# Performance work log

Measured on AMD Instinct MI355X. Metric: run time of the kernel, lower is better.

The kernel has to match this reference:

```python
import jax, jax.numpy as jnp
import numpy as np

OBS, ACT, H = 64, 16, 64
T, B = 512, 4096


def _orth(key, shape):
    # orthogonal init like nn.init.orthogonal_ (gain 1 for predict; capture uses
    # gain sqrt(2) via init_ wrapper, but predict re-inits to plain orthogonal).
    a = jax.random.normal(key, shape, dtype=jnp.float32)
    q, r = jnp.linalg.qr(a if shape[0] >= shape[1] else a.T)
    q = q * jnp.sign(jnp.diag(r))
    return q if shape[0] >= shape[1] else q.T


def setup_inputs() -> dict:
    key = jax.random.key(0)
    ks = jax.random.split(key, 10)
    g2 = np.sqrt(2.0).astype(np.float32)
    inp = {
        "x": jax.random.normal(ks[0], (T, B, OBS), dtype=jnp.float32),
        "h": jax.random.normal(ks[1], (1, B, H), dtype=jnp.float32),
        "g": jax.random.uniform(ks[2], (T, B, 1), dtype=jnp.float32),
        "a": jax.random.normal(ks[3], (T, B, ACT), dtype=jnp.float32),
        # capture MLP: Linear(obs->H), tanh, Linear(H->H), tanh  (gain sqrt(2))
        "Wc1": g2 * _orth(ks[4], (OBS, H)),
        "bc1": jnp.zeros((H,), jnp.float32),
        "Wc2": g2 * _orth(ks[5], (H, H)),
        "bc2": jnp.zeros((H,), jnp.float32),
        # predict (Dynamics): Linear(H+ACT->H), tanh, Linear(H->H), tanh (gain 1)
        "Wp1": _orth(ks[6], (H + ACT, H)),
        "bp1": jnp.zeros((H,), jnp.float32),
        "Wp2": _orth(ks[7], (H, H)),
        "bp2": jnp.zeros((H,), jnp.float32),
    }
    return inp


def reference(x, h, g, a, Wc1, bc1, Wc2, bc2, Wp1, bp1, Wp2, bp2):
    # capture branch has no recurrent dependence -> compute for all t at once
    z1_all = jnp.tanh(jnp.tanh(x @ Wc1 + bc1) @ Wc2 + bc2)  # [T, B, H]

    def step(h_prev, inp):  # h_prev: [B, H]
        z1_t, g_t, a_t = inp
        ha = jnp.concatenate([h_prev, a_t], axis=-1)  # [B, H+ACT]
        z2 = jnp.tanh(jnp.tanh(ha @ Wp1 + bp1) @ Wp2 + bp2)
        h_new = (1.0 - g_t) * z1_t + g_t * z2
        return h_new, h_new

    h_final, outs = jax.lax.scan(step, h[0], (z1_all, g, a))
    capt = z1_all.reshape(-1, z1_all.shape[-1])  # torch.cat over [B,H] chunks -> [T*B, H]
    return outs, h_final[None], capt
```

## Files before the change

kernel.cpp:

```cpp
#include <hip/hip_runtime.h>
#include <hip/hip_bf16.h>

#define T_STEPS 512
#define BATCH   4096
#define ACT     16
#define HDIM    64

typedef short s8v __attribute__((ext_vector_type(8)));
typedef float f4v __attribute__((ext_vector_type(4)));

#define MFMA16(A, B, C) __builtin_amdgcn_mfma_f32_16x16x32_bf16((A), (B), (C), 0, 0, 0)

__device__ __forceinline__ unsigned pkbf(float a, float b) {
    unsigned r;
    asm("v_cvt_pk_bf16_f32 %0, %1, %2" : "=v"(r) : "v"(a), "v"(b));
    return r;
}
__device__ __forceinline__ float hi16f(unsigned p) { return __builtin_bit_cast(float, p & 0xFFFF0000u); }
__device__ __forceinline__ unsigned short f2bf(float f) {
    unsigned u = __builtin_bit_cast(unsigned, f);
    u += 0x7FFFu + ((u >> 16) & 1u);
    return (unsigned short)(u >> 16);
}
__device__ __forceinline__ float bf2f(unsigned short b) {
    return __builtin_bit_cast(float, ((unsigned)b) << 16);
}
__device__ __forceinline__ float ftanh(float x) {
    float e = __expf(2.0f * x);
    return fmaf(-2.0f, __builtin_amdgcn_rcpf(e + 1.0f), 1.0f);
}
struct i4x { int a, b, c, d; };
__device__ __forceinline__ s8v pack4(f4v v) {
    unsigned p0 = pkbf(v[0], v[0]); float r0 = v[0] - hi16f(p0);
    unsigned p1 = pkbf(v[1], v[1]); float r1 = v[1] - hi16f(p1);
    unsigned p2 = pkbf(v[2], v[2]); float r2 = v[2] - hi16f(p2);
    unsigned p3 = pkbf(v[3], v[3]); float r3 = v[3] - hi16f(p3);
    i4x w{(int)pkbf(v[0], r0), (int)pkbf(v[1], r1), (int)pkbf(v[2], r2), (int)pkbf(v[3], r3)};
    return __builtin_bit_cast(s8v, w);
}
#define BAR() do { \
    asm volatile("s_waitcnt lgkmcnt(0)" ::: "memory"); \
    __builtin_amdgcn_s_barrier(); \
    asm volatile("" ::: "memory"); \
} while (0)

__global__ __launch_bounds__(256, 1) void capture_k(
    const float* __restrict__ x,
    const float* __restrict__ Wc1, const float* __restrict__ bc1,
    const float* __restrict__ Wc2, const float* __restrict__ bc2,
    float* __restrict__ capt)
{
    const int tid = threadIdx.x;
    const int l   = tid & 63;
    const int m   = l & 15;
    const int q   = l >> 4;
    const int gw  = blockIdx.x * 4 + (tid >> 6);
    const int NW  = 1024;
    const long NT = (long)T_STEPS * BATCH / 16;

    s8v C1[4][4], C2h[4][4], C2l[4][4];
    f4v d1v[4], d2v[4];
    #pragma unroll
    for (int T = 0; T < 4; ++T) {
        #pragma unroll
        for (int f = 0; f < 4; ++f) {
            #pragma unroll
            for (int e = 0; e < 8; ++e) {
                const int j = f * 16 + q * 4 + (e >> 1);
                C1[T][f][e] = (short)f2bf(Wc1[j * 64 + 16 * T + m]);
                float v2 = Wc2[j * 64 + 16 * T + m];
                unsigned short h2 = f2bf(v2);
                C2h[T][f][e] = (short)h2;
                C2l[T][f][e] = (short)f2bf(v2 - bf2f(h2));
            }
        }
        d1v[T] = *(const f4v*)&bc1[16 * T + 4 * q];
        d2v[T] = *(const f4v*)&bc2[16 * T + 4 * q];
    }

    long tile = gw;
    if (tile >= NT) return;
    f4v XC[4];
    #pragma unroll
    for (int f = 0; f < 4; ++f)
        XC[f] = *(const f4v*)&x[(tile * 16 + m) * 64 + 16 * f + 4 * q];

    for (; tile < NT; tile += NW) {
        const long nxt = (tile + NW < NT) ? tile + NW : tile;
        f4v XN[4];
        #pragma unroll
        for (int f = 0; f < 4; ++f)
            XN[f] = *(const f4v*)&x[(nxt * 16 + m) * 64 + 16 * f + 4 * q];

        s8v xf[4];
        #pragma unroll
        for (int f = 0; f < 4; ++f) xf[f] = pack4(XC[f]);

        s8v tcf[4];
        #pragma unroll
        for (int T = 0; T < 4; ++T) {
            f4v u0 = d1v[T];
            f4v u1 = {0.f, 0.f, 0.f, 0.f};
            u0 = MFMA16(C1[T][0], xf[0], u0);
            u1 = MFMA16(C1[T][1], xf[1], u1);
            u0 = MFMA16(C1[T][2], xf[2], u0);
            u1 = MFMA16(C1[T][3], xf[3], u1);
            f4v tv;
            #pragma unroll
            for (int r = 0; r < 4; ++r) tv[r] = ftanh(u0[r] + u1[r]);
            tcf[T] = pack4(tv);
        }
        #pragma unroll
        for (int T = 0; T < 4; ++T) {
            f4v c0 = d2v[T];
            f4v c1 = {0.f, 0.f, 0.f, 0.f}, c2 = c1, c3 = c1;
            c0 = MFMA16(C2h[T][0], tcf[0], c0);
            c1 = MFMA16(C2h[T][1], tcf[1], c1);
            c2 = MFMA16(C2h[T][2], tcf[2], c2);
            c3 = MFMA16(C2h[T][3], tcf[3], c3);
            c0 = MFMA16(C2l[T][0], tcf[0], c0);
            c1 = MFMA16(C2l[T][1], tcf[1], c1);
            c2 = MFMA16(C2l[T][2], tcf[2], c2);
            c3 = MFMA16(C2l[T][3], tcf[3], c3);
            f4v zv;
            #pragma unroll
            for (int r = 0; r < 4; ++r) zv[r] = ftanh((c0[r] + c1[r]) + (c2[r] + c3[r]));
            *(f4v*)&capt[(tile * 16 + m) * 64 + 16 * T + 4 * q] = zv;
        }
        #pragma unroll
        for (int f = 0; f < 4; ++f) XC[f] = XN[f];
    }
}

__global__ __launch_bounds__(256, 1) void recur_k(
    const float* __restrict__ h0, const float* __restrict__ g,
    const float* __restrict__ a,  const float* __restrict__ Wp1,
    const float* __restrict__ bp1, const float* __restrict__ Wp2,
    const float* __restrict__ bp2, const float* __restrict__ z1,
    float* __restrict__ outs, float* __restrict__ hfin)
{
    __shared__ s8v hx[4][64];
    __shared__ s8v t1x[4][64];

    const int tid = threadIdx.x;
    const int T   = tid >> 6;
    const int l   = tid & 63;
    const int m   = l & 15;
    const int q   = l >> 4;
    const int b0  = blockIdx.x << 4;

    s8v W1[5], W2h[4], W2l[4];
    #pragma unroll
    for (int f = 0; f < 4; ++f) {
        #pragma unroll
        for (int e = 0; e < 8; ++e) {
            const int j = f * 16 + q * 4 + (e >> 1);
            W1[f][e] = (short)f2bf(Wp1[j * 64 + 16 * T + m]);
            float v2 = Wp2[j * 64 + 16 * T + m];
            unsigned short h2 = f2bf(v2);
            W2h[f][e] = (short)h2;
            W2l[f][e] = (short)f2bf(v2 - bf2f(h2));
        }
    }
    #pragma unroll
    for (int e = 0; e < 8; ++e) {
        const int j = 64 + q * 4 + (e >> 1);
        W1[4][e] = (short)f2bf(Wp1[j * 64 + 16 * T + m]);
    }
    const f4v b1v = *(const f4v*)&bp1[16 * T + 4 * q];
    const f4v b2v = *(const f4v*)&bp2[16 * T + 4 * q];

    const long zoff = (long)(b0 + m) * 64 + 16 * T + 4 * q;
    const long aoff = (long)(b0 + m) * ACT + 4 * q;
    const long goff = (long)(b0 + m);

    {
        f4v h0v = *(const f4v*)&h0[zoff];
        hx[T][l] = pack4(h0v);
    }
    f4v zP0 = *(const f4v*)&z1[0 * (long)BATCH * 64 + zoff];
    f4v zP1 = *(const f4v*)&z1[1 * (long)BATCH * 64 + zoff];
    f4v zP2 = *(const f4v*)&z1[2 * (long)BATCH * 64 + zoff];
    f4v zP3 = *(const f4v*)&z1[3 * (long)BATCH * 64 + zoff];
    f4v aP0 = *(const f4v*)&a[0 * (long)BATCH * ACT + aoff];
    f4v aP1 = *(const f4v*)&a[1 * (long)BATCH * ACT + aoff];
    f4v aP2 = *(const f4v*)&a[2 * (long)BATCH * ACT + aoff];
    f4v aP3 = *(const f4v*)&a[3 * (long)BATCH * ACT + aoff];
    float gP0 = g[0 * (long)BATCH + goff];
    float gP1 = g[1 * (long)BATCH + goff];
    float gP2 = g[2 * (long)BATCH + goff];
    float gP3 = g[3 * (long)BATCH + goff];

    float* outp = &outs[zoff];
    f4v hl = {0.f, 0.f, 0.f, 0.f};
    __syncthreads();

#define RSTEP(tt, ZP, AP, GP) {                                               \
                                    \
    s8v hf0 = hx[0][l];                                                       \
    s8v hf1 = hx[1][l];                                                       \
    s8v hf2 = hx[2][l];                                                       \
    s8v hf3 = hx[3][l];                                                       \
    s8v afr = pack4(AP);                                                      \
    f4v p0 = b1v;                                                             \
    f4v p1 = {0.f, 0.f, 0.f, 0.f}, p2 = p1;                                   \
    p0 = MFMA16(W1[0], hf0, p0);                                              \
    p1 = MFMA16(W1[1], hf1, p1);                                              \
    p2 = MFMA16(W1[2], hf2, p2);                                              \
    p0 = MFMA16(W1[3], hf3, p0);                                              \
    p1 = MFMA16(W1[4], afr, p1);                                              \
    f4v tv;                                                                   \
    _Pragma("unroll")                                                         \
    for (int r = 0; r < 4; ++r) tv[r] = ftanh((p0[r] + p1[r]) + p2[r]);       \
    t1x[T][l] = pack4(tv);                                                    \
    BAR();                                                                    \
                                           \
    s8v tf0 = t1x[0][l];                                                      \
    s8v tf1 = t1x[1][l];                                                      \
    s8v tf2 = t1x[2][l];                                                      \
    s8v tf3 = t1x[3][l];                                                      \
    f4v c0 = b2v;                                                             \
    f4v c1 = {0.f, 0.f, 0.f, 0.f}, c2 = c1, c3 = c1;                          \
    c0 = MFMA16(W2h[0], tf0, c0);                                             \
    c1 = MFMA16(W2h[1], tf1, c1);                                             \
    c2 = MFMA16(W2h[2], tf2, c2);                                             \
    c3 = MFMA16(W2h[3], tf3, c3);                                             \
    c0 = MFMA16(W2l[0], tf0, c0);                                             \
    c1 = MFMA16(W2l[1], tf1, c1);                                             \
    c2 = MFMA16(W2l[2], tf2, c2);                                             \
    c3 = MFMA16(W2l[3], tf3, c3);                                             \
    f4v hv;                                                                   \
    _Pragma("unroll")                                                         \
    for (int r = 0; r < 4; ++r) {                                             \
        float z2 = ftanh((c0[r] + c1[r]) + (c2[r] + c3[r]));                  \
        hv[r] = fmaf(GP, z2 - ZP[r], ZP[r]);                                  \
    }                                                                         \
    *(f4v*)outp = hv;                                                         \
    outp += (long)BATCH * HDIM;                                               \
    hl = hv;                                                                  \
    hx[T][l] = pack4(hv);                                                     \
                                     \
    {                                                                         \
        const long tn = ((tt) + 4 < T_STEPS) ? (tt) + 4 : T_STEPS - 1;        \
        ZP = *(const f4v*)&z1[tn * (long)BATCH * 64 + zoff];                  \
        AP = *(const f4v*)&a[tn * (long)BATCH * ACT + aoff];                  \
        GP = g[tn * (long)BATCH + goff];                                      \
    }                                                                         \
    BAR();                                                                    \
}

    for (int t = 0; t < T_STEPS; t += 4) {
        RSTEP(t + 0, zP0, aP0, gP0);
        RSTEP(t + 1, zP1, aP1, gP1);
        RSTEP(t + 2, zP2, aP2, gP2);
        RSTEP(t + 3, zP3, aP3, gP3);
    }
#undef RSTEP

    *(f4v*)&hfin[zoff] = hl;
}

extern "C" void kernel_launch(void* const* d_in, const int* in_sizes, int n_in,
                              void* d_out, int out_size, void* d_ws, size_t ws_size,
                              hipStream_t stream) {
    const float* x   = (const float*)d_in[0];
    const float* h0  = (const float*)d_in[1];
    const float* g   = (const float*)d_in[2];
    const float* a   = (const float*)d_in[3];
    const float* Wc1 = (const float*)d_in[4];
    const float* bc1 = (const float*)d_in[5];
    const float* Wc2 = (const float*)d_in[6];
    const float* bc2 = (const float*)d_in[7];
    const float* Wp1 = (const float*)d_in[8];
    const float* bp1 = (const float*)d_in[9];
    const float* Wp2 = (const float*)d_in[10];
    const float* bp2 = (const float*)d_in[11];

    float* outs = (float*)d_out;
    float* hfin = outs + (long)T_STEPS * BATCH * HDIM;
    float* capt = hfin + (long)BATCH * HDIM;

    capture_k<<<256, 256, 0, stream>>>(x, Wc1, bc1, Wc2, bc2, capt);
    recur_k<<<BATCH / 16, 256, 0, stream>>>(h0, g, a, Wp1, bp1, Wp2, bp2, capt, outs, hfin);
}
```

Baseline: 605.0 us.

## Fuse capture MLP and recurrence into one warp-specialized kernel with LDS flag handoff

Merges the two kernels into one 512-thread block. Four producer waves compute the capture MLP and pass z1 through a 4-deep LDS ring, so z1 is no longer re-read from global memory by the recurrence. Four consumer waves each compute the full first predict layer redundantly, which removes the mid-step barrier, and they double-buffer h. The two wave groups synchronize with volatile LDS flags and s_sleep spin-waits instead of block barriers. The risks are spin-wait overhead, more registers per wave, and the correctness of the flag ordering.

```diff
diff --git a/kernel.cpp b/kernel.cpp
--- a/kernel.cpp
+++ b/kernel.cpp
@@ -38,226 +38,242 @@
     i4x w{(int)pkbf(v[0], r0), (int)pkbf(v[1], r1), (int)pkbf(v[2], r2), (int)pkbf(v[3], r3)};
     return __builtin_bit_cast(s8v, w);
 }
-#define BAR() do { \
-    asm volatile("s_waitcnt lgkmcnt(0)" ::: "memory"); \
-    __builtin_amdgcn_s_barrier(); \
-    asm volatile("" ::: "memory"); \
-} while (0)
-
-__global__ __launch_bounds__(256, 1) void capture_k(
-    const float* __restrict__ x,
+
+__global__ __launch_bounds__(512, 2) void fused_cell(
+    const float* __restrict__ x,  const float* __restrict__ h0,
+    const float* __restrict__ g,  const float* __restrict__ a,
     const float* __restrict__ Wc1, const float* __restrict__ bc1,
     const float* __restrict__ Wc2, const float* __restrict__ bc2,
-    float* __restrict__ capt)
+    const float* __restrict__ Wp1, const float* __restrict__ bp1,
+    const float* __restrict__ Wp2, const float* __restrict__ bp2,
+    float* __restrict__ outs, float* __restrict__ hfin, float* __restrict__ capt)
 {
+    __shared__ s8v   hx[2][4][64];
+    __shared__ float zr[4][16][68];
+    __shared__ int   flg[16];
+
     const int tid = threadIdx.x;
-    const int l   = tid & 63;
-    const int m   = l & 15;
-    const int q   = l >> 4;
-    const int gw  = blockIdx.x * 4 + (tid >> 6);
-    const int NW  = 1024;
-    const long NT = (long)T_STEPS * BATCH / 16;
-
-    s8v C1[4][4], C2h[4][4], C2l[4][4];
-    f4v d1v[4], d2v[4];
-    #pragma unroll
-    for (int T = 0; T < 4; ++T) {
+    const int wv  = tid >> 6;
+    const int T   = wv & 3;
+    const bool capw = wv >= 4;
+    const int l  = tid & 63;
+    const int m  = l & 15;
+    const int q  = l >> 4;
+    const int b0 = blockIdx.x << 4;
+
+    volatile int* pf = (volatile int*)flg;
+    volatile int* zf = (volatile int*)(flg + 8);
+    if (tid < 16) flg[tid] = 0;
+
+    if (!capw) {
+        s8v W1[4][5];
+        s8v W2h[4], W2l[4];
+        f4v b1v[4], b2v;
         #pragma unroll
-        for (int f = 0; f < 4; ++f) {
+        for (int o = 0; o < 4; ++o) {
+            #pragma unroll
+            for (int f = 0; f < 4; ++f)
+                #pragma unroll
+                for (int e = 0; e < 8; ++e) {
+                    const int j = f * 16 + q * 4 + (e >> 1);
+                    W1[o][f][e] = (short)f2bf(Wp1[j * 64 + 16 * o + m]);
+                }
+            #pragma unroll
+            for (int e = 0; e < 8; ++e) {
+                const int j = 64 + q * 4 + (e >> 1);
+                W1[o][4][e] = (short)f2bf(Wp1[j * 64 + 16 * o + m]);
+            }
+            b1v[o] = *(const f4v*)&bp1[16 * o + 4 * q];
+        }
+        #pragma unroll
+        for (int f = 0; f < 4; ++f)
             #pragma unroll
             for (int e = 0; e < 8; ++e) {
                 const int j = f * 16 + q * 4 + (e >> 1);
-                C1[T][f][e] = (short)f2bf(Wc1[j * 64 + 16 * T + m]);
-                float v2 = Wc2[j * 64 + 16 * T + m];
+                float v2 = Wp2[j * 64 + 16 * T + m];
                 unsigned short h2 = f2bf(v2);
-                C2h[T][f][e] = (short)h2;
-                C2l[T][f][e] = (short)f2bf(v2 - bf2f(h2));
+                W2h[f][e] = (short)h2;
+                W2l[f][e] = (short)f2bf(v2 - bf2f(h2));
             }
-        }
-        d1v[T] = *(const f4v*)&bc1[16 * T + 4 * q];
-        d2v[T] = *(const f4v*)&bc2[16 * T + 4 * q];
-    }
-
-    long tile = gw;
-    if (tile >= NT) return;
-    f4v XC[4];
-    #pragma unroll
-    for (int f = 0; f < 4; ++f)
-        XC[f] = *(const f4v*)&x[(tile * 16 + m) * 64 + 16 * f + 4 * q];
-
-    for (; tile < NT; tile += NW) {
-        const long nxt = (tile + NW < NT) ? tile + NW : tile;
-        f4v XN[4];
-        #pragma unroll
-        for (int f = 0; f < 4; ++f)
-            XN[f] = *(const f4v*)&x[(nxt * 16 + m) * 64 + 16 * f + 4 * q];
-
-        s8v xf[4];
-        #pragma unroll
-        for (int f = 0; f < 4; ++f) xf[f] = pack4(XC[f]);
-
-        s8v tcf[4];
-        #pragma unroll
-        for (int T = 0; T < 4; ++T) {
-            f4v u0 = d1v[T];
-            f4v u1 = {0.f, 0.f, 0.f, 0.f};
-            u0 = MFMA16(C1[T][0], xf[0], u0);
-            u1 = MFMA16(C1[T][1], xf[1], u1);
-            u0 = MFMA16(C1[T][2], xf[2], u0);
-            u1 = MFMA16(C1[T][3], xf[3], u1);
-            f4v tv;
-            #pragma unroll
-            for (int r = 0; r < 4; ++r) tv[r] = ftanh(u0[r] + u1[r]);
-            tcf[T] = pack4(tv);
-        }
-        #pragma unroll
-        for (int T = 0; T < 4; ++T) {
-            f4v c0 = d2v[T];
-            f4v c1 = {0.f, 0.f, 0.f, 0.f}, c2 = c1, c3 = c1;
-            c0 = MFMA16(C2h[T][0], tcf[0], c0);
-            c1 = MFMA16(C2h[T][1], tcf[1], c1);
-            c2 = MFMA16(C2h[T][2], tcf[2], c2);
-            c3 = MFMA16(C2h[T][3], tcf[3], c3);
-            c0 = MFMA16(C2l[T][0], tcf[0], c0);
-            c1 = MFMA16(C2l[T][1], tcf[1], c1);
-            c2 = MFMA16(C2l[T][2], tcf[2], c2);
-            c3 = MFMA16(C2l[T][3], tcf[3], c3);
-            f4v zv;
-            #pragma unroll
-            for (int r = 0; r < 4; ++r) zv[r] = ftanh((c0[r] + c1[r]) + (c2[r] + c3[r]));
-            *(f4v*)&capt[(tile * 16 + m) * 64 + 16 * T + 4 * q] = zv;
-        }
-        #pragma unroll
-        for (int f = 0; f < 4; ++f) XC[f] = XN[f];
-    }
-}
-
-__global__ __launch_bounds__(256, 1) void recur_k(
-    const float* __restrict__ h0, const float* __restrict__ g,
-    const float* __restrict__ a,  const float* __restrict__ Wp1,
-    const float* __restrict__ bp1, const float* __restrict__ Wp2,
-    const float* __restrict__ bp2, const float* __restrict__ z1,
-    float* __restrict__ outs, float* __restrict__ hfin)
-{
-    __shared__ s8v hx[4][64];
-    __shared__ s8v t1x[4][64];
-
-    const int tid = threadIdx.x;
-    const int T   = tid >> 6;
-    const int l   = tid & 63;
-    const int m   = l & 15;
-    const int q   = l >> 4;
-    const int b0  = blockIdx.x << 4;
-
-    s8v W1[5], W2h[4], W2l[4];
-    #pragma unroll
-    for (int f = 0; f < 4; ++f) {
-        #pragma unroll
-        for (int e = 0; e < 8; ++e) {
-            const int j = f * 16 + q * 4 + (e >> 1);
-            W1[f][e] = (short)f2bf(Wp1[j * 64 + 16 * T + m]);
-            float v2 = Wp2[j * 64 + 16 * T + m];
-            unsigned short h2 = f2bf(v2);
-            W2h[f][e] = (short)h2;
-            W2l[f][e] = (short)f2bf(v2 - bf2f(h2));
-        }
-    }
-    #pragma unroll
-    for (int e = 0; e < 8; ++e) {
-        const int j = 64 + q * 4 + (e >> 1);
-        W1[4][e] = (short)f2bf(Wp1[j * 64 + 16 * T + m]);
-    }
-    const f4v b1v = *(const f4v*)&bp1[16 * T + 4 * q];
-    const f4v b2v = *(const f4v*)&bp2[16 * T + 4 * q];
-
-    const long zoff = (long)(b0 + m) * 64 + 16 * T + 4 * q;
-    const long aoff = (long)(b0 + m) * ACT + 4 * q;
-    const long goff = (long)(b0 + m);
-
-    {
-        f4v h0v = *(const f4v*)&h0[zoff];
-        hx[T][l] = pack4(h0v);
-    }
-    f4v zP0 = *(const f4v*)&z1[0 * (long)BATCH * 64 + zoff];
-    f4v zP1 = *(const f4v*)&z1[1 * (long)BATCH * 64 + zoff];
-    f4v zP2 = *(const f4v*)&z1[2 * (long)BATCH * 64 + zoff];
-    f4v zP3 = *(const f4v*)&z1[3 * (long)BATCH * 64 + zoff];
-    f4v aP0 = *(const f4v*)&a[0 * (long)BATCH * ACT + aoff];
-    f4v aP1 = *(const f4v*)&a[1 * (long)BATCH * ACT + aoff];
-    f4v aP2 = *(const f4v*)&a[2 * (long)BATCH * ACT + aoff];
-    f4v aP3 = *(const f4v*)&a[3 * (long)BATCH * ACT + aoff];
-    float gP0 = g[0 * (long)BATCH + goff];
-    float gP1 = g[1 * (long)BATCH + goff];
-    float gP2 = g[2 * (long)BATCH + goff];
-    float gP3 = g[3 * (long)BATCH + goff];
-
-    float* outp = &outs[zoff];
-    f4v hl = {0.f, 0.f, 0.f, 0.f};
-    __syncthreads();
-
-#define RSTEP(tt, ZP, AP, GP) {                                               \
-                                    \
-    s8v hf0 = hx[0][l];                                                       \
-    s8v hf1 = hx[1][l];                                                       \
-    s8v hf2 = hx[2][l];                                                       \
-    s8v hf3 = hx[3][l];                                                       \
-    s8v afr = pack4(AP);                                                      \
-    f4v p0 = b1v;                                                             \
-    f4v p1 = {0.f, 0.f, 0.f, 0.f}, p2 = p1;                                   \
-    p0 = MFMA16(W1[0], hf0, p0);                                              \
-    p1 = MFMA16(W1[1], hf1, p1);                                              \
-    p2 = MFMA16(W1[2], hf2, p2);                                              \
-    p0 = MFMA16(W1[3], hf3, p0);                                              \
-    p1 = MFMA16(W1[4], afr, p1);                                              \
-    f4v tv;                                                                   \
+        b2v = *(const f4v*)&bp2[16 * T + 4 * q];
+
+        hx[0][T][l] = pack4(*(const f4v*)&h0[(long)(b0 + m) * 64 + 16 * T + 4 * q]);
+
+        const long aoff = (long)(b0 + m) * ACT + 4 * q;
+        const long goff = (long)(b0 + m);
+        f4v aA = *(const f4v*)&a[aoff];
+        f4v aB = *(const f4v*)&a[(long)BATCH * ACT + aoff];
+        float gA = g[goff];
+        float gB = g[(long)BATCH + goff];
+        const float* apA = a + (long)2 * BATCH * ACT + aoff;
+        const float* apB = a + (long)3 * BATCH * ACT + aoff;
+        const float* gpA = g + (long)2 * BATCH + goff;
+        const float* gpB = g + (long)3 * BATCH + goff;
+
+        float* outp = &outs[(long)(b0 + m) * 64 + 16 * T + 4 * q];
+        f4v hl = {0.f, 0.f, 0.f, 0.f};
+
+        __syncthreads();
+        __builtin_amdgcn_s_setprio(1);
+
+#define L1T(o, dst) {                                                         \
+    f4v p0 = b1v[o];                                                          \
+    f4v p1 = {0.f, 0.f, 0.f, 0.f};                                            \
+    p0 = MFMA16(W1[o][0], hf0, p0);                                           \
+    p1 = MFMA16(W1[o][1], hf1, p1);                                           \
+    p0 = MFMA16(W1[o][2], hf2, p0);                                           \
+    p1 = MFMA16(W1[o][3], hf3, p1);                                           \
+    p0 = MFMA16(W1[o][4], afr, p0);                                           \
+    f4v tv_;                                                                  \
     _Pragma("unroll")                                                         \
-    for (int r = 0; r < 4; ++r) tv[r] = ftanh((p0[r] + p1[r]) + p2[r]);       \
-    t1x[T][l] = pack4(tv);                                                    \
-    BAR();                                                                    \
-                                           \
-    s8v tf0 = t1x[0][l];                                                      \
-    s8v tf1 = t1x[1][l];                                                      \
-    s8v tf2 = t1x[2][l];                                                      \
-    s8v tf3 = t1x[3][l];                                                      \
+    for (int r = 0; r < 4; ++r) tv_[r] = ftanh(p0[r] + p1[r]);                \
+    dst = pack4(tv_);                                                         \
+}
+
+#define RSTEP(tt, AC, GC, APTR, GPTR) do {                                    \
+    const int t_ = (tt);                                                      \
+    const f4v aC_ = AC; const float gC_ = GC;                                 \
+    while (pf[0] < t_ || pf[1] < t_ || pf[2] < t_ || pf[3] < t_ ||            \
+           zf[0] <= t_ || zf[1] <= t_ || zf[2] <= t_ || zf[3] <= t_)          \
+        __builtin_amdgcn_s_sleep(1);                                          \
+    asm volatile("" ::: "memory");                                            \
+    const f4v z1v = *(const f4v*)&zr[t_ & 3][m][16 * T + 4 * q];              \
+    const s8v* hb = &hx[t_ & 1][0][0];                                        \
+    const s8v hf0 = hb[l];                                                    \
+    const s8v hf1 = hb[64 + l];                                               \
+    const s8v hf2 = hb[128 + l];                                              \
+    const s8v hf3 = hb[192 + l];                                              \
+    const s8v afr = pack4(aC_);                                               \
+    AC = *(const f4v*)APTR; if (t_ + 4 < T_STEPS) APTR += 2 * BATCH * ACT;    \
+    GC = *GPTR;             if (t_ + 4 < T_STEPS) GPTR += 2 * BATCH;          \
+    s8v tcf0, tcf1, tcf2, tcf3;                                               \
+    L1T(0, tcf0) L1T(1, tcf1) L1T(2, tcf2) L1T(3, tcf3)                       \
     f4v c0 = b2v;                                                             \
     f4v c1 = {0.f, 0.f, 0.f, 0.f}, c2 = c1, c3 = c1;                          \
-    c0 = MFMA16(W2h[0], tf0, c0);                                             \
-    c1 = MFMA16(W2h[1], tf1, c1);                                             \
-    c2 = MFMA16(W2h[2], tf2, c2);                                             \
-    c3 = MFMA16(W2h[3], tf3, c3);                                             \
-    c0 = MFMA16(W2l[0], tf0, c0);                                             \
-    c1 = MFMA16(W2l[1], tf1, c1);                                             \
-    c2 = MFMA16(W2l[2], tf2, c2);                                             \
-    c3 = MFMA16(W2l[3], tf3, c3);                                             \
+    c0 = MFMA16(W2h[0], tcf0, c0); c1 = MFMA16(W2h[1], tcf1, c1);             \
+    c2 = MFMA16(W2h[2], tcf2, c2); c3 = MFMA16(W2h[3], tcf3, c3);             \
+    c0 = MFMA16(W2l[0], tcf0, c0); c1 = MFMA16(W2l[1], tcf1, c1);             \
+    c2 = MFMA16(W2l[2], tcf2, c2); c3 = MFMA16(W2l[3], tcf3, c3);             \
     f4v hv;                                                                   \
     _Pragma("unroll")                                                         \
     for (int r = 0; r < 4; ++r) {                                             \
         float z2 = ftanh((c0[r] + c1[r]) + (c2[r] + c3[r]));                  \
-        hv[r] = fmaf(GP, z2 - ZP[r], ZP[r]);                                  \
+        hv[r] = fmaf(gC_, z2 - z1v[r], z1v[r]);                               \
     }                                                                         \
-    *(f4v*)outp = hv;                                                         \
-    outp += (long)BATCH * HDIM;                                               \
+    *(f4v*)outp = hv; outp += (long)BATCH * HDIM;                             \
     hl = hv;                                                                  \
-    hx[T][l] = pack4(hv);                                                     \
-                                     \
-    {                                                                         \
-        const long tn = ((tt) + 4 < T_STEPS) ? (tt) + 4 : T_STEPS - 1;        \
-        ZP = *(const f4v*)&z1[tn * (long)BATCH * 64 + zoff];                  \
-        AP = *(const f4v*)&a[tn * (long)BATCH * ACT + aoff];                  \
-        GP = g[tn * (long)BATCH + goff];                                      \
+    hx[(t_ + 1) & 1][T][l] = pack4(hv);                                       \
+    asm volatile("s_waitcnt lgkmcnt(0)" ::: "memory");                        \
+    if (l == 0) pf[T] = t_ + 1;                                               \
+} while (0)
+
+        for (int t = 0; t < T_STEPS; t += 2) {
+            RSTEP(t,     aA, gA, apA, gpA);
+            RSTEP(t + 1, aB, gB, apB, gpB);
+        }
+#undef RSTEP
+#undef L1T
+
+        *(f4v*)&hfin[(long)(b0 + m) * 64 + 16 * T + 4 * q] = hl;
+
+    } else {
+        s8v C1[4][4];
+        s8v C2h[4], C2l[4];
+        f4v d1v[4], d2v;
+        #pragma unroll
+        for (int o = 0; o < 4; ++o) {
+            #pragma unroll
+            for (int f = 0; f < 4; ++f)
+                #pragma unroll
+                for (int e = 0; e < 8; ++e) {
+                    const int j = f * 16 + q * 4 + (e >> 1);
+                    C1[o][f][e] = (short)f2bf(Wc1[j * 64 + 16 * o + m]);
+                }
+            d1v[o] = *(const f4v*)&bc1[16 * o + 4 * q];
+        }
+        #pragma unroll
+        for (int f = 0; f < 4; ++f)
+            #pragma unroll
+            for (int e = 0; e < 8; ++e) {
+                const int j = f * 16 + q * 4 + (e >> 1);
+                float v2 = Wc2[j * 64 + 16 * T + m];
+                unsigned short h2 = f2bf(v2);
+                C2h[f][e] = (short)h2;
+                C2l[f][e] = (short)f2bf(v2 - bf2f(h2));
+            }
+        d2v = *(const f4v*)&bc2[16 * T + 4 * q];
+
+        const float* bx = x + (long)(b0 + m) * 64 + 4 * q;
+        f4v XA0 = *(const f4v*)(bx);
+        f4v XA1 = *(const f4v*)(bx + 16);
+        f4v XA2 = *(const f4v*)(bx + 32);
+        f4v XA3 = *(const f4v*)(bx + 48);
+        const float* bx1 = bx + (long)BATCH * HDIM;
+        f4v XB0 = *(const f4v*)(bx1);
+        f4v XB1 = *(const f4v*)(bx1 + 16);
+        f4v XB2 = *(const f4v*)(bx1 + 32);
+        f4v XB3 = *(const f4v*)(bx1 + 48);
+        const float* xpA = bx + (long)2 * BATCH * HDIM;
+        const float* xpB = bx + (long)3 * BATCH * HDIM;
+
+        float* cp = &capt[(long)(b0 + m) * 64 + 16 * T + 4 * q];
+
+        __syncthreads();
+
+#define CL1T(o, dst) {                                                        \
+    f4v p0 = d1v[o];                                                          \
+    f4v p1 = {0.f, 0.f, 0.f, 0.f};                                            \
+    p0 = MFMA16(C1[o][0], xf0, p0);                                           \
+    p1 = MFMA16(C1[o][1], xf1, p1);                                           \
+    p0 = MFMA16(C1[o][2], xf2, p0);                                           \
+    p1 = MFMA16(C1[o][3], xf3, p1);                                           \
+    f4v tv_;                                                                  \
+    _Pragma("unroll")                                                         \
+    for (int r = 0; r < 4; ++r) tv_[r] = ftanh(p0[r] + p1[r]);                \
+    dst = pack4(tv_);                                                         \
+}
+
+#define CSTEP(tt, X0, X1, X2, X3, XPTR) do {                                  \
+    const int t_ = (tt);                                                      \
+    if (t_ >= 4) {                                                            \
+        const int want = t_ - 3;                                              \
+        while (pf[0] < want || pf[1] < want || pf[2] < want || pf[3] < want)  \
+            __builtin_amdgcn_s_sleep(1);                                      \
+        asm volatile("" ::: "memory");                                        \
     }                                                                         \
-    BAR();                                                                    \
-}
-
-    for (int t = 0; t < T_STEPS; t += 4) {
-        RSTEP(t + 0, zP0, aP0, gP0);
-        RSTEP(t + 1, zP1, aP1, gP1);
-        RSTEP(t + 2, zP2, aP2, gP2);
-        RSTEP(t + 3, zP3, aP3, gP3);
+    const s8v xf0 = pack4(X0);                                                \
+    const s8v xf1 = pack4(X1);                                                \
+    const s8v xf2 = pack4(X2);                                                \
+    const s8v xf3 = pack4(X3);                                                \
+    X0 = *(const f4v*)(XPTR);                                                 \
+    X1 = *(const f4v*)(XPTR + 16);                                            \
+    X2 = *(const f4v*)(XPTR + 32);                                            \
+    X3 = *(const f4v*)(XPTR + 48);                                            \
+    if (t_ + 4 < T_STEPS) XPTR += (long)2 * BATCH * HDIM;                     \
+    s8v tcf0, tcf1, tcf2, tcf3;                                               \
+    CL1T(0, tcf0) CL1T(1, tcf1) CL1T(2, tcf2) CL1T(3, tcf3)                   \
+    f4v c0 = d2v;                                                             \
+    f4v c1 = {0.f, 0.f, 0.f, 0.f}, c2 = c1, c3 = c1;                          \
+    c0 = MFMA16(C2h[0], tcf0, c0); c1 = MFMA16(C2h[1], tcf1, c1);             \
+    c2 = MFMA16(C2h[2], tcf2, c2); c3 = MFMA16(C2h[3], tcf3, c3);             \
+    c0 = MFMA16(C2l[0], tcf0, c0); c1 = MFMA16(C2l[1], tcf1, c1);             \
+    c2 = MFMA16(C2l[2], tcf2, c2); c3 = MFMA16(C2l[3], tcf3, c3);             \
+    f4v zv;                                                                   \
+    _Pragma("unroll")                                                         \
+    for (int r = 0; r < 4; ++r) zv[r] = ftanh((c0[r] + c1[r]) + (c2[r] + c3[r])); \
+    *(f4v*)&zr[t_ & 3][m][16 * T + 4 * q] = zv;                               \
+    *(f4v*)cp = zv; cp += (long)BATCH * HDIM;                                 \
+    asm volatile("s_waitcnt lgkmcnt(0)" ::: "memory");                        \
+    if (l == 0) zf[T] = t_ + 1;                                               \
+} while (0)
+
+        for (int t = 0; t < T_STEPS; t += 2) {
+            CSTEP(t,     XA0, XA1, XA2, XA3, xpA);
+            CSTEP(t + 1, XB0, XB1, XB2, XB3, xpB);
+        }
+#undef CSTEP
+#undef CL1T
     }
-#undef RSTEP
-
-    *(f4v*)&hfin[zoff] = hl;
 }
 
 extern "C" void kernel_launch(void* const* d_in, const int* in_sizes, int n_in,
@@ -280,6 +296,6 @@
     float* hfin = outs + (long)T_STEPS * BATCH * HDIM;
     float* capt = hfin + (long)BATCH * HDIM;
 
-    capture_k<<<256, 256, 0, stream>>>(x, Wc1, bc1, Wc2, bc2, capt);
-    recur_k<<<BATCH / 16, 256, 0, stream>>>(h0, g, a, Wp1, bp1, Wp2, bp2, capt, outs, hfin);
-}
+    fused_cell<<<BATCH / 16, 512, 0, stream>>>(
+        x, h0, g, a, Wc1, bc1, Wc2, bc2, Wp1, bp1, Wp2, bp2, outs, hfin, capt);
+}
```

New measurement: 1.003 ms. 1.66x slower.

## Process two batch tiles per recurrent block and double capture grid

Applied to the files above, without the earlier changes.

The recurrent kernel now has each block handle 32 batch rows as two independent 16-row chains. Their MFMAs are interleaved so each barrier and the tanh latency are shared across twice the work, and the launch uses half as many blocks (128). The prefetch distance drops from four steps to two to keep register pressure manageable. The capture kernel moves to 512 blocks with launch bounds allowing 2 blocks per CU, which raises occupancy but may increase register pressure. The risks are that 128 blocks leave many CUs idle and that the shorter prefetch distance exposes more load latency.

```diff
diff --git a/kernel.cpp b/kernel.cpp
--- a/kernel.cpp
+++ b/kernel.cpp
@@ -44,7 +44,7 @@
     asm volatile("" ::: "memory"); \
 } while (0)
 
-__global__ __launch_bounds__(256, 1) void capture_k(
+__global__ __launch_bounds__(256, 2) void capture_k(
     const float* __restrict__ x,
     const float* __restrict__ Wc1, const float* __restrict__ bc1,
     const float* __restrict__ Wc2, const float* __restrict__ bc2,
@@ -55,7 +55,7 @@
     const int m   = l & 15;
     const int q   = l >> 4;
     const int gw  = blockIdx.x * 4 + (tid >> 6);
-    const int NW  = 1024;
+    const int NW  = 2048;
     const long NT = (long)T_STEPS * BATCH / 16;
 
     s8v C1[4][4], C2h[4][4], C2l[4][4];
@@ -139,19 +139,19 @@
     const float* __restrict__ bp2, const float* __restrict__ z1,
     float* __restrict__ outs, float* __restrict__ hfin)
 {
-    __shared__ s8v hx[4][64];
-    __shared__ s8v t1x[4][64];
+    __shared__ s8v hx[2][4][64];
+    __shared__ s8v t1x[2][4][64];
 
     const int tid = threadIdx.x;
     const int T   = tid >> 6;
     const int l   = tid & 63;
     const int m   = l & 15;
     const int q   = l >> 4;
-    const int b0  = blockIdx.x << 4;
+    const int b0  = blockIdx.x << 5;
 
     s8v W1[5], W2h[4], W2l[4];
     #pragma unroll
-    for (int f = 0; f < 4; ++f) {
+    for (int f = 0; f < 4; ++f)
         #pragma unroll
         for (int e = 0; e < 8; ++e) {
             const int j = f * 16 + q * 4 + (e >> 1);
@@ -161,7 +161,6 @@
             W2h[f][e] = (short)h2;
             W2l[f][e] = (short)f2bf(v2 - bf2f(h2));
         }
-    }
     #pragma unroll
     for (int e = 0; e < 8; ++e) {
         const int j = 64 + q * 4 + (e >> 1);
@@ -170,94 +169,114 @@
     const f4v b1v = *(const f4v*)&bp1[16 * T + 4 * q];
     const f4v b2v = *(const f4v*)&bp2[16 * T + 4 * q];
 
-    const long zoff = (long)(b0 + m) * 64 + 16 * T + 4 * q;
-    const long aoff = (long)(b0 + m) * ACT + 4 * q;
-    const long goff = (long)(b0 + m);
-
-    {
-        f4v h0v = *(const f4v*)&h0[zoff];
-        hx[T][l] = pack4(h0v);
-    }
-    f4v zP0 = *(const f4v*)&z1[0 * (long)BATCH * 64 + zoff];
-    f4v zP1 = *(const f4v*)&z1[1 * (long)BATCH * 64 + zoff];
-    f4v zP2 = *(const f4v*)&z1[2 * (long)BATCH * 64 + zoff];
-    f4v zP3 = *(const f4v*)&z1[3 * (long)BATCH * 64 + zoff];
-    f4v aP0 = *(const f4v*)&a[0 * (long)BATCH * ACT + aoff];
-    f4v aP1 = *(const f4v*)&a[1 * (long)BATCH * ACT + aoff];
-    f4v aP2 = *(const f4v*)&a[2 * (long)BATCH * ACT + aoff];
-    f4v aP3 = *(const f4v*)&a[3 * (long)BATCH * ACT + aoff];
-    float gP0 = g[0 * (long)BATCH + goff];
-    float gP1 = g[1 * (long)BATCH + goff];
-    float gP2 = g[2 * (long)BATCH + goff];
-    float gP3 = g[3 * (long)BATCH + goff];
-
-    float* outp = &outs[zoff];
-    f4v hl = {0.f, 0.f, 0.f, 0.f};
+    const long zf0 = (long)(b0 + m) * 64 + 16 * T + 4 * q;
+    const long zf1 = zf0 + 16 * 64;
+    const long af0_ = (long)(b0 + m) * ACT + 4 * q;
+    const long af1_ = af0_ + 16 * ACT;
+    const long gf0 = (long)(b0 + m);
+    const long gf1 = gf0 + 16;
+
+    hx[0][T][l] = pack4(*(const f4v*)&h0[zf0]);
+    hx[1][T][l] = pack4(*(const f4v*)&h0[zf1]);
+
+    f4v z0A = *(const f4v*)&z1[zf0];
+    f4v z0B = *(const f4v*)&z1[(long)BATCH * 64 + zf0];
+    f4v z1A = *(const f4v*)&z1[zf1];
+    f4v z1B = *(const f4v*)&z1[(long)BATCH * 64 + zf1];
+    f4v a0A = *(const f4v*)&a[af0_];
+    f4v a0B = *(const f4v*)&a[(long)BATCH * ACT + af0_];
+    f4v a1A = *(const f4v*)&a[af1_];
+    f4v a1B = *(const f4v*)&a[(long)BATCH * ACT + af1_];
+    float g0A = g[gf0], g0B = g[(long)BATCH + gf0];
+    float g1A = g[gf1], g1B = g[(long)BATCH + gf1];
+
+    float* out0 = &outs[zf0];
+    float* out1 = &outs[zf1];
+    f4v hl0 = {0.f, 0.f, 0.f, 0.f}, hl1 = hl0;
     __syncthreads();
 
-#define RSTEP(tt, ZP, AP, GP) {                                               \
-                                    \
-    s8v hf0 = hx[0][l];                                                       \
-    s8v hf1 = hx[1][l];                                                       \
-    s8v hf2 = hx[2][l];                                                       \
-    s8v hf3 = hx[3][l];                                                       \
-    s8v afr = pack4(AP);                                                      \
-    f4v p0 = b1v;                                                             \
-    f4v p1 = {0.f, 0.f, 0.f, 0.f}, p2 = p1;                                   \
-    p0 = MFMA16(W1[0], hf0, p0);                                              \
-    p1 = MFMA16(W1[1], hf1, p1);                                              \
-    p2 = MFMA16(W1[2], hf2, p2);                                              \
-    p0 = MFMA16(W1[3], hf3, p0);                                              \
-    p1 = MFMA16(W1[4], afr, p1);                                              \
-    f4v tv;                                                                   \
-    _Pragma("unroll")                                                         \
-    for (int r = 0; r < 4; ++r) tv[r] = ftanh((p0[r] + p1[r]) + p2[r]);       \
-    t1x[T][l] = pack4(tv);                                                    \
-    BAR();                                                                    \
-                                           \
-    s8v tf0 = t1x[0][l];                                                      \
-    s8v tf1 = t1x[1][l];                                                      \
-    s8v tf2 = t1x[2][l];                                                      \
-    s8v tf3 = t1x[3][l];                                                      \
-    f4v c0 = b2v;                                                             \
-    f4v c1 = {0.f, 0.f, 0.f, 0.f}, c2 = c1, c3 = c1;                          \
-    c0 = MFMA16(W2h[0], tf0, c0);                                             \
-    c1 = MFMA16(W2h[1], tf1, c1);                                             \
-    c2 = MFMA16(W2h[2], tf2, c2);                                             \
-    c3 = MFMA16(W2h[3], tf3, c3);                                             \
-    c0 = MFMA16(W2l[0], tf0, c0);                                             \
-    c1 = MFMA16(W2l[1], tf1, c1);                                             \
-    c2 = MFMA16(W2l[2], tf2, c2);                                             \
-    c3 = MFMA16(W2l[3], tf3, c3);                                             \
-    f4v hv;                                                                   \
+#define RSTEP(tt, Z0, A0, G0, Z1v, A1, G1) do {                               \
+                                   \
+    const s8v h00 = hx[0][0][l];                                              \
+    const s8v h01 = hx[0][1][l];                                              \
+    const s8v h02 = hx[0][2][l];                                              \
+    const s8v h03 = hx[0][3][l];                                              \
+    const s8v h10 = hx[1][0][l];                                              \
+    const s8v h11 = hx[1][1][l];                                              \
+    const s8v h12 = hx[1][2][l];                                              \
+    const s8v h13 = hx[1][3][l];                                              \
+    const s8v af0 = pack4(A0);                                                \
+    const s8v af1 = pack4(A1);                                                \
+    f4v p00 = b1v, p10 = b1v;                                                 \
+    f4v p01 = {0.f, 0.f, 0.f, 0.f}, p02 = p01, p11 = p01, p12 = p01;          \
+    p00 = MFMA16(W1[0], h00, p00);  p10 = MFMA16(W1[0], h10, p10);            \
+    p01 = MFMA16(W1[1], h01, p01);  p11 = MFMA16(W1[1], h11, p11);            \
+    p02 = MFMA16(W1[2], h02, p02);  p12 = MFMA16(W1[2], h12, p12);            \
+    p00 = MFMA16(W1[3], h03, p00);  p10 = MFMA16(W1[3], h13, p10);            \
+    p01 = MFMA16(W1[4], af0, p01);  p11 = MFMA16(W1[4], af1, p11);            \
+    f4v tv0, tv1;                                                             \
     _Pragma("unroll")                                                         \
     for (int r = 0; r < 4; ++r) {                                             \
-        float z2 = ftanh((c0[r] + c1[r]) + (c2[r] + c3[r]));                  \
-        hv[r] = fmaf(GP, z2 - ZP[r], ZP[r]);                                  \
+        tv0[r] = ftanh((p00[r] + p01[r]) + p02[r]);                           \
+        tv1[r] = ftanh((p10[r] + p11[r]) + p12[r]);                           \
     }                                                                         \
-    *(f4v*)outp = hv;                                                         \
-    outp += (long)BATCH * HDIM;                                               \
-    hl = hv;                                                                  \
-    hx[T][l] = pack4(hv);                                                     \
-                                     \
+    t1x[0][T][l] = pack4(tv0);                                                \
+    t1x[1][T][l] = pack4(tv1);                                                \
+    BAR();                                                                    \
+                           \
+    const s8v t00 = t1x[0][0][l];                                             \
+    const s8v t01 = t1x[0][1][l];                                             \
+    const s8v t02 = t1x[0][2][l];                                             \
+    const s8v t03 = t1x[0][3][l];                                             \
+    const s8v t10 = t1x[1][0][l];                                             \
+    const s8v t11 = t1x[1][1][l];                                             \
+    const s8v t12 = t1x[1][2][l];                                             \
+    const s8v t13 = t1x[1][3][l];                                             \
+    f4v c00 = b2v, c10 = b2v;                                                 \
+    f4v c01 = {0.f, 0.f, 0.f, 0.f}, c02 = c01, c03 = c01;                     \
+    f4v c11 = c01, c12 = c01, c13 = c01;                                      \
+    c00 = MFMA16(W2h[0], t00, c00);  c10 = MFMA16(W2h[0], t10, c10);          \
+    c01 = MFMA16(W2h[1], t01, c01);  c11 = MFMA16(W2h[1], t11, c11);          \
+    c02 = MFMA16(W2h[2], t02, c02);  c12 = MFMA16(W2h[2], t12, c12);          \
+    c03 = MFMA16(W2h[3], t03, c03);  c13 = MFMA16(W2h[3], t13, c13);          \
+    c00 = MFMA16(W2l[0], t00, c00);  c10 = MFMA16(W2l[0], t10, c10);          \
+    c01 = MFMA16(W2l[1], t01, c01);  c11 = MFMA16(W2l[1], t11, c11);          \
+    c02 = MFMA16(W2l[2], t02, c02);  c12 = MFMA16(W2l[2], t12, c12);          \
+    c03 = MFMA16(W2l[3], t03, c03);  c13 = MFMA16(W2l[3], t13, c13);          \
+    f4v hv0, hv1;                                                             \
+    _Pragma("unroll")                                                         \
+    for (int r = 0; r < 4; ++r) {                                             \
+        float z20 = ftanh((c00[r] + c01[r]) + (c02[r] + c03[r]));             \
+        float z21 = ftanh((c10[r] + c11[r]) + (c12[r] + c13[r]));             \
+        hv0[r] = fmaf(G0, z20 - Z0[r], Z0[r]);                                \
+        hv1[r] = fmaf(G1, z21 - Z1v[r], Z1v[r]);                              \
+    }                                                                         \
+    *(f4v*)out0 = hv0;  out0 += (long)BATCH * HDIM;                           \
+    *(f4v*)out1 = hv1;  out1 += (long)BATCH * HDIM;                           \
+    hl0 = hv0; hl1 = hv1;                                                     \
+    hx[0][T][l] = pack4(hv0);                                                 \
+    hx[1][T][l] = pack4(hv1);                                                 \
+                                          \
     {                                                                         \
-        const long tn = ((tt) + 4 < T_STEPS) ? (tt) + 4 : T_STEPS - 1;        \
-        ZP = *(const f4v*)&z1[tn * (long)BATCH * 64 + zoff];                  \
-        AP = *(const f4v*)&a[tn * (long)BATCH * ACT + aoff];                  \
-        GP = g[tn * (long)BATCH + goff];                                      \
+        const long tn = ((tt) + 2 < T_STEPS) ? (tt) + 2 : T_STEPS - 1;        \
+        Z0  = *(const f4v*)&z1[tn * (long)BATCH * 64 + zf0];                  \
+        Z1v = *(const f4v*)&z1[tn * (long)BATCH * 64 + zf1];                  \
+        A0  = *(const f4v*)&a[tn * (long)BATCH * ACT + af0_];                 \
+        A1  = *(const f4v*)&a[tn * (long)BATCH * ACT + af1_];                 \
+        G0  = g[tn * (long)BATCH + gf0];                                      \
+        G1  = g[tn * (long)BATCH + gf1];                                      \
     }                                                                         \
     BAR();                                                                    \
-}
-
-    for (int t = 0; t < T_STEPS; t += 4) {
-        RSTEP(t + 0, zP0, aP0, gP0);
-        RSTEP(t + 1, zP1, aP1, gP1);
-        RSTEP(t + 2, zP2, aP2, gP2);
-        RSTEP(t + 3, zP3, aP3, gP3);
+} while (0)
+
+    for (int t = 0; t < T_STEPS; t += 2) {
+        RSTEP(t,     z0A, a0A, g0A, z1A, a1A, g1A);
+        RSTEP(t + 1, z0B, a0B, g0B, z1B, a1B, g1B);
     }
 #undef RSTEP
 
-    *(f4v*)&hfin[zoff] = hl;
+    *(f4v*)&hfin[zf0] = hl0;
+    *(f4v*)&hfin[zf1] = hl1;
 }
 
 extern "C" void kernel_launch(void* const* d_in, const int* in_sizes, int n_in,
@@ -280,6 +299,6 @@
     float* hfin = outs + (long)T_STEPS * BATCH * HDIM;
     float* capt = hfin + (long)BATCH * HDIM;
 
-    capture_k<<<256, 256, 0, stream>>>(x, Wc1, bc1, Wc2, bc2, capt);
-    recur_k<<<BATCH / 16, 256, 0, stream>>>(h0, g, a, Wp1, bp1, Wp2, bp2, capt, outs, hfin);
-}
+    capture_k<<<512, 256, 0, stream>>>(x, Wc1, bc1, Wc2, bc2, capt);
+    recur_k<<<BATCH / 32, 256, 0, stream>>>(h0, g, a, Wp1, bp1, Wp2, bp2, capt, outs, hfin);
+}
```

New measurement: 1.160 ms. 91.7% more time.

## Compute full first layer redundantly per wave to drop one barrier per step

Applied to the files above, without the earlier changes.

Each wave now computes all four 16-column tiles of the first predict layer (holding all W1 fragments in registers) instead of one tile, so the intermediate activation never goes through shared memory. This removes one of the two block barriers per recurrent step, and the hidden state buffer is double-buffered by step parity so a single barrier suffices. The trade-off is four times the layer-1 MFMA and tanh work per wave and higher register pressure from the extra weight fragments.

```diff
diff --git a/kernel.cpp b/kernel.cpp
--- a/kernel.cpp
+++ b/kernel.cpp
@@ -139,8 +139,7 @@
     const float* __restrict__ bp2, const float* __restrict__ z1,
     float* __restrict__ outs, float* __restrict__ hfin)
 {
-    __shared__ s8v hx[4][64];
-    __shared__ s8v t1x[4][64];
+    __shared__ s8v hx[2][4][64];
 
     const int tid = threadIdx.x;
     const int T   = tid >> 6;
@@ -149,35 +148,43 @@
     const int q   = l >> 4;
     const int b0  = blockIdx.x << 4;
 
-    s8v W1[5], W2h[4], W2l[4];
-    #pragma unroll
-    for (int f = 0; f < 4; ++f) {
+    s8v W1a[4][5];
+    f4v b1v[4];
+    #pragma unroll
+    for (int o = 0; o < 4; ++o) {
+        #pragma unroll
+        for (int f = 0; f < 4; ++f)
+            #pragma unroll
+            for (int e = 0; e < 8; ++e) {
+                const int j = f * 16 + q * 4 + (e >> 1);
+                W1a[o][f][e] = (short)f2bf(Wp1[j * 64 + 16 * o + m]);
+            }
+        #pragma unroll
+        for (int e = 0; e < 8; ++e) {
+            const int j = 64 + q * 4 + (e >> 1);
+            W1a[o][4][e] = (short)f2bf(Wp1[j * 64 + 16 * o + m]);
+        }
+        b1v[o] = *(const f4v*)&bp1[16 * o + 4 * q];
+    }
+    s8v W2h[4], W2l[4];
+    #pragma unroll
+    for (int f = 0; f < 4; ++f)
         #pragma unroll
         for (int e = 0; e < 8; ++e) {
             const int j = f * 16 + q * 4 + (e >> 1);
-            W1[f][e] = (short)f2bf(Wp1[j * 64 + 16 * T + m]);
             float v2 = Wp2[j * 64 + 16 * T + m];
             unsigned short h2 = f2bf(v2);
             W2h[f][e] = (short)h2;
             W2l[f][e] = (short)f2bf(v2 - bf2f(h2));
         }
-    }
-    #pragma unroll
-    for (int e = 0; e < 8; ++e) {
-        const int j = 64 + q * 4 + (e >> 1);
-        W1[4][e] = (short)f2bf(Wp1[j * 64 + 16 * T + m]);
-    }
-    const f4v b1v = *(const f4v*)&bp1[16 * T + 4 * q];
     const f4v b2v = *(const f4v*)&bp2[16 * T + 4 * q];
 
     const long zoff = (long)(b0 + m) * 64 + 16 * T + 4 * q;
     const long aoff = (long)(b0 + m) * ACT + 4 * q;
     const long goff = (long)(b0 + m);
 
-    {
-        f4v h0v = *(const f4v*)&h0[zoff];
-        hx[T][l] = pack4(h0v);
-    }
+    hx[0][T][l] = pack4(*(const f4v*)&h0[zoff]);
+
     f4v zP0 = *(const f4v*)&z1[0 * (long)BATCH * 64 + zoff];
     f4v zP1 = *(const f4v*)&z1[1 * (long)BATCH * 64 + zoff];
     f4v zP2 = *(const f4v*)&z1[2 * (long)BATCH * 64 + zoff];
@@ -186,49 +193,41 @@
     f4v aP1 = *(const f4v*)&a[1 * (long)BATCH * ACT + aoff];
     f4v aP2 = *(const f4v*)&a[2 * (long)BATCH * ACT + aoff];
     f4v aP3 = *(const f4v*)&a[3 * (long)BATCH * ACT + aoff];
-    float gP0 = g[0 * (long)BATCH + goff];
-    float gP1 = g[1 * (long)BATCH + goff];
-    float gP2 = g[2 * (long)BATCH + goff];
-    float gP3 = g[3 * (long)BATCH + goff];
+    float gP0 = g[0 * (long)BATCH + goff], gP1 = g[1 * (long)BATCH + goff];
+    float gP2 = g[2 * (long)BATCH + goff], gP3 = g[3 * (long)BATCH + goff];
 
     float* outp = &outs[zoff];
     f4v hl = {0.f, 0.f, 0.f, 0.f};
     __syncthreads();
 
-#define RSTEP(tt, ZP, AP, GP) {                                               \
-                                    \
-    s8v hf0 = hx[0][l];                                                       \
-    s8v hf1 = hx[1][l];                                                       \
-    s8v hf2 = hx[2][l];                                                       \
-    s8v hf3 = hx[3][l];                                                       \
-    s8v afr = pack4(AP);                                                      \
-    f4v p0 = b1v;                                                             \
+#define L1T(o, dst) {                                                         \
+    f4v p0 = b1v[o];                                                          \
     f4v p1 = {0.f, 0.f, 0.f, 0.f}, p2 = p1;                                   \
-    p0 = MFMA16(W1[0], hf0, p0);                                              \
-    p1 = MFMA16(W1[1], hf1, p1);                                              \
-    p2 = MFMA16(W1[2], hf2, p2);                                              \
-    p0 = MFMA16(W1[3], hf3, p0);                                              \
-    p1 = MFMA16(W1[4], afr, p1);                                              \
-    f4v tv;                                                                   \
+    p0 = MFMA16(W1a[o][0], hf0, p0);                                          \
+    p1 = MFMA16(W1a[o][1], hf1, p1);                                          \
+    p2 = MFMA16(W1a[o][2], hf2, p2);                                          \
+    p0 = MFMA16(W1a[o][3], hf3, p0);                                          \
+    p1 = MFMA16(W1a[o][4], afr, p1);                                          \
+    f4v tv_;                                                                  \
     _Pragma("unroll")                                                         \
-    for (int r = 0; r < 4; ++r) tv[r] = ftanh((p0[r] + p1[r]) + p2[r]);       \
-    t1x[T][l] = pack4(tv);                                                    \
-    BAR();                                                                    \
-                                           \
-    s8v tf0 = t1x[0][l];                                                      \
-    s8v tf1 = t1x[1][l];                                                      \
-    s8v tf2 = t1x[2][l];                                                      \
-    s8v tf3 = t1x[3][l];                                                      \
+    for (int r = 0; r < 4; ++r) tv_[r] = ftanh((p0[r] + p1[r]) + p2[r]);      \
+    dst = pack4(tv_);                                                         \
+}
+
+#define RSTEP(tt, PAR, ZP, AP, GP) do {                                       \
+    const s8v hf0 = hx[PAR][0][l];                                            \
+    const s8v hf1 = hx[PAR][1][l];                                            \
+    const s8v hf2 = hx[PAR][2][l];                                            \
+    const s8v hf3 = hx[PAR][3][l];                                            \
+    const s8v afr = pack4(AP);                                                \
+    s8v t1f0, t1f1, t1f2, t1f3;                                               \
+    L1T(0, t1f0) L1T(1, t1f1) L1T(2, t1f2) L1T(3, t1f3)                       \
     f4v c0 = b2v;                                                             \
     f4v c1 = {0.f, 0.f, 0.f, 0.f}, c2 = c1, c3 = c1;                          \
-    c0 = MFMA16(W2h[0], tf0, c0);                                             \
-    c1 = MFMA16(W2h[1], tf1, c1);                                             \
-    c2 = MFMA16(W2h[2], tf2, c2);                                             \
-    c3 = MFMA16(W2h[3], tf3, c3);                                             \
-    c0 = MFMA16(W2l[0], tf0, c0);                                             \
-    c1 = MFMA16(W2l[1], tf1, c1);                                             \
-    c2 = MFMA16(W2l[2], tf2, c2);                                             \
-    c3 = MFMA16(W2l[3], tf3, c3);                                             \
+    c0 = MFMA16(W2h[0], t1f0, c0); c1 = MFMA16(W2h[1], t1f1, c1);             \
+    c2 = MFMA16(W2h[2], t1f2, c2); c3 = MFMA16(W2h[3], t1f3, c3);             \
+    c0 = MFMA16(W2l[0], t1f0, c0); c1 = MFMA16(W2l[1], t1f1, c1);             \
+    c2 = MFMA16(W2l[2], t1f2, c2); c3 = MFMA16(W2l[3], t1f3, c3);             \
     f4v hv;                                                                   \
     _Pragma("unroll")                                                         \
     for (int r = 0; r < 4; ++r) {                                             \
@@ -238,8 +237,7 @@
     *(f4v*)outp = hv;                                                         \
     outp += (long)BATCH * HDIM;                                               \
     hl = hv;                                                                  \
-    hx[T][l] = pack4(hv);                                                     \
-                                     \
+    hx[PAR ^ 1][T][l] = pack4(hv);                                            \
     {                                                                         \
         const long tn = ((tt) + 4 < T_STEPS) ? (tt) + 4 : T_STEPS - 1;        \
         ZP = *(const f4v*)&z1[tn * (long)BATCH * 64 + zoff];                  \
@@ -247,15 +245,16 @@
         GP = g[tn * (long)BATCH + goff];                                      \
     }                                                                         \
     BAR();                                                                    \
-}
+} while (0)
 
     for (int t = 0; t < T_STEPS; t += 4) {
-        RSTEP(t + 0, zP0, aP0, gP0);
-        RSTEP(t + 1, zP1, aP1, gP1);
-        RSTEP(t + 2, zP2, aP2, gP2);
-        RSTEP(t + 3, zP3, aP3, gP3);
+        RSTEP(t + 0, 0, zP0, aP0, gP0);
+        RSTEP(t + 1, 1, zP1, aP1, gP1);
+        RSTEP(t + 2, 0, zP2, aP2, gP2);
+        RSTEP(t + 3, 1, zP3, aP3, gP3);
     }
 #undef RSTEP
+#undef L1T
 
     *(f4v*)&hfin[zoff] = hl;
 }
```

Measured after the change: 769.3 us. 27.2% more time.
